# Kernel tuning notes

Hardware: AMD Instinct MI355X
Metric: run time of the kernel (lower is better)

The kernel has to match this reference:

```python
import jax, jax.numpy as jnp
import numpy as np

NUM_SYMBOLS = 100000
EMBED_DIM = 256
DIM = 2 * EMBED_DIM          # 512
NUM_HEADS = 4
HEAD_DIM = DIM // NUM_HEADS  # 128
N = 100                      # hard-coded neighbor count in source
EPS = 1e-5


def layernorm(x, g, b):
    mu = jnp.mean(x, axis=-1, keepdims=True)
    var = jnp.var(x, axis=-1, keepdims=True)
    return (x - mu) * jax.lax.rsqrt(var + EPS) * g + b


def setup_inputs() -> dict:
    key = jax.random.key(0)
    ks = jax.random.split(key, 12)
    B, FEW = 512, 2
    connections = jax.random.randint(ks[0], (B, FEW, N, 2), 0, NUM_SYMBOLS)
    mask = jax.random.randint(ks[1], (B * FEW, N, N), 0, 2).astype(jnp.int32)
    s = 0.02
    emb = jax.random.normal(ks[2], (NUM_SYMBOLS + 1, EMBED_DIM), jnp.float32) * s
    qkv_w = jax.random.normal(ks[3], (3 * DIM, DIM), jnp.float32) * s
    qkv_b = jnp.zeros((3 * DIM,), jnp.float32)
    proj_w = jax.random.normal(ks[4], (DIM, DIM), jnp.float32) * s
    proj_b = jnp.zeros((DIM,), jnp.float32)
    ln1_g = jnp.ones((DIM,), jnp.float32); ln1_b = jnp.zeros((DIM,), jnp.float32)
    ln2_g = jnp.ones((DIM,), jnp.float32); ln2_b = jnp.zeros((DIM,), jnp.float32)
    fc_w = jax.random.normal(ks[5], (DIM // 2, DIM), jnp.float32) * s
    fc_b = jnp.zeros((DIM // 2,), jnp.float32)
    return {"connections": connections, "mask": mask, "emb": emb,
            "qkv_w": qkv_w, "qkv_b": qkv_b, "proj_w": proj_w, "proj_b": proj_b,
            "ln1_g": ln1_g, "ln1_b": ln1_b, "ln2_g": ln2_g, "ln2_b": ln2_b,
            "fc_w": fc_w, "fc_b": fc_b}


def reference(connections, mask, emb, qkv_w, qkv_b, proj_w, proj_b,
              ln1_g, ln1_b, ln2_g, ln2_b, fc_w, fc_b):
    # embedding gathers for (relation, entity) pairs
    rel = emb[connections[..., 0]]          # [B, few, N, E]
    ent = emb[connections[..., 1]]          # [B, few, N, E]
    x = jnp.concatenate([rel, ent], axis=-1).reshape(-1, N, DIM)  # [BN, N, C]
    m = mask.reshape(-1, N, N)

    xn = layernorm(x, ln1_g, ln1_b)
    qkv = xn @ qkv_w.T + qkv_b              # [BN, N, 3C]
    BN = xn.shape[0]
    qkv = qkv.reshape(BN, N, 3, NUM_HEADS, HEAD_DIM).transpose(2, 0, 3, 1, 4)
    q, k, v = qkv[0], qkv[1], qkv[2]        # [BN, H, N, hd]

    scale = HEAD_DIM ** -0.5
    attn = jnp.einsum('bhnd,bhmd->bhnm', q, k) * scale
    attn = jnp.where(m[:, None] == 0, -1e9, attn)
    attn = jax.nn.softmax(attn, axis=-1)    # [BN, H, N, N]

    y = jnp.einsum('bhnm,bhmd->bhnd', attn, v)
    y = y.transpose(0, 2, 1, 3).reshape(BN, N, DIM)
    y = y @ proj_w.T + proj_b               # [BN, N, C]

    # attn.mean(dim=2): mean over query axis -> [BN, H, N]; bmm with y
    wc = jnp.einsum('bhn,bnc->bhc', attn.mean(axis=2), y)   # [BN, H, C]
    out = layernorm(wc, ln2_g, ln2_b) @ fc_w.T + fc_b       # [BN, H, C//2]
    return out
```

## Files before the change

### kernel.cpp

```cpp
#include <hip/hip_runtime.h>
#include <stdint.h>

typedef __attribute__((ext_vector_type(8))) short bf16x8;
typedef __attribute__((ext_vector_type(4))) float f32x4;
typedef __attribute__((ext_vector_type(4))) unsigned int u32x4;
typedef __attribute__((ext_vector_type(4))) unsigned short u16x4;

typedef const void __attribute__((address_space(1))) gvoid_t;
typedef void __attribute__((address_space(3))) lvoid_t;

__device__ __forceinline__ unsigned short f2bf(float f) {
  union { float f; unsigned int u; } v; v.f = f;
  unsigned int u = v.u;
  u += 0x7fffu + ((u >> 16) & 1u);
  return (unsigned short)(u >> 16);
}
__device__ __forceinline__ float bf2f(unsigned short h) {
  union { unsigned int u; float f; } v; v.u = ((unsigned int)h) << 16;
  return v.f;
}
__device__ __forceinline__ void load_lds16(const void* g, void* l) {
  __builtin_amdgcn_global_load_lds((gvoid_t*)g, (lvoid_t*)l, 16, 0, 0);
}

#define GATE4() asm volatile("s_waitcnt vmcnt(4)" ::: "memory")
#define GATE0() asm volatile("s_waitcnt vmcnt(0)" ::: "memory")
#define BARRIER()                    \
  do {                               \
    asm volatile("" ::: "memory");   \
    __builtin_amdgcn_s_barrier();    \
    asm volatile("" ::: "memory");   \
  } while (0)

__global__ __launch_bounds__(256) void k_cvt(const float* __restrict__ src,
                                             unsigned short* __restrict__ dst, int n) {
  int i = blockIdx.x * 256 + threadIdx.x;
  if (i < n) dst[i] = f2bf(src[i]);
}

__global__ __launch_bounds__(256) void k_maskpack(const int* __restrict__ mask,
                                                  unsigned int* __restrict__ bm) {
  const int lane = threadIdx.x & 63;
  const int wv = (blockIdx.x << 2) + (threadIdx.x >> 6);
  const int r0 = wv * 16;
  for (int i = 0; i < 16; ++i) {
    const int r = r0 + i;
    const size_t base = (size_t)r * 100;
    const int c0 = mask[base + lane];
    int c1 = 0;
    if (lane < 36) c1 = mask[base + 64 + lane];
    const unsigned long long b0 = __ballot(c0 != 0);
    const unsigned long long b1 = __ballot(c1 != 0);
    if (lane == 0) {
      u32x4 v;
      v[0] = (unsigned int)b0; v[1] = (unsigned int)(b0 >> 32);
      v[2] = (unsigned int)b1; v[3] = (unsigned int)(b1 >> 32);
      *(u32x4*)(bm + (size_t)r * 4) = v;
    }
  }
}

__global__ __launch_bounds__(256) void k_gather_ln(const int* __restrict__ conn,
                                                   const float* __restrict__ emb,
                                                   const float* __restrict__ g1,
                                                   const float* __restrict__ b1,
                                                   unsigned short* __restrict__ xn,
                                                   int row0) {
  const int lane = threadIdx.x & 63;
  const int wid = threadIdx.x >> 6;
  const int rloc = blockIdx.x * 4 + wid;
  const int row = row0 + rloc;
  const int rel = conn[row * 2 + 0];
  const int ent = conn[row * 2 + 1];
  const float4 r4 = *(const float4*)(emb + (size_t)rel * 256 + lane * 4);
  const float4 e4 = *(const float4*)(emb + (size_t)ent * 256 + lane * 4);
  float rv[4] = {r4.x, r4.y, r4.z, r4.w};
  float ev[4] = {e4.x, e4.y, e4.z, e4.w};
  float s = 0.f, ss = 0.f;
#pragma unroll
  for (int j = 0; j < 4; ++j) { s += rv[j] + ev[j]; ss += rv[j] * rv[j] + ev[j] * ev[j]; }
#pragma unroll
  for (int d = 1; d < 64; d <<= 1) { s += __shfl_xor(s, d, 64); ss += __shfl_xor(ss, d, 64); }
  const float mu = s * (1.f / 512.f);
  const float var = ss * (1.f / 512.f) - mu * mu;
  const float rs = rsqrtf(var + 1e-5f);
  const float4 ga = *(const float4*)(g1 + lane * 4);
  const float4 gb = *(const float4*)(g1 + 256 + lane * 4);
  const float4 ba = *(const float4*)(b1 + lane * 4);
  const float4 bb = *(const float4*)(b1 + 256 + lane * 4);
  float gav[4] = {ga.x, ga.y, ga.z, ga.w}, gbv[4] = {gb.x, gb.y, gb.z, gb.w};
  float bav[4] = {ba.x, ba.y, ba.z, ba.w}, bbv[4] = {bb.x, bb.y, bb.z, bb.w};
  u16x4 o0, o1;
#pragma unroll
  for (int j = 0; j < 4; ++j) {
    o0[j] = f2bf((rv[j] - mu) * rs * gav[j] + bav[j]);
    o1[j] = f2bf((ev[j] - mu) * rs * gbv[j] + bbv[j]);
  }
  unsigned short* orow = xn + (size_t)rloc * 512;
  *(u16x4*)(orow + lane * 4) = o0;
  *(u16x4*)(orow + 256 + lane * 4) = o1;
}

template <typename CT>
__global__ __launch_bounds__(256) void k_gemm3(const unsigned short* __restrict__ A,
                                               const unsigned short* __restrict__ W,
                                               const float* __restrict__ bias,
                                               CT* __restrict__ C,
                                               int N, int K, int ntiles, int nwg) {
  __shared__ __align__(16) unsigned short ldsA[3][128 * 32];
  __shared__ __align__(16) unsigned short ldsB[3][128 * 32];

  const int orig = blockIdx.x;
  const int q = nwg >> 3, r = nwg & 7;
  const int xcd = orig & 7, idx = orig >> 3;
  const int wg = (xcd < r ? xcd * (q + 1) : r * (q + 1) + (xcd - r) * q) + idx;
  const int mtile = wg / ntiles, ntile = wg % ntiles;

  const int t = threadIdx.x, lane = t & 63, wid = t >> 6;
  const int wm = wid >> 1, wn = wid & 1;
  const size_t Abase = (size_t)mtile * 128 * K;
  const size_t Wbase = (size_t)ntile * 128 * K;
  const int NT = K >> 5;

  f32x4 acc[4][4];
#pragma unroll
  for (int i = 0; i < 4; ++i)
#pragma unroll
    for (int j = 0; j < 4; ++j) acc[i][j] = (f32x4){0.f, 0.f, 0.f, 0.f};

  const int sr0 = t >> 2;
  auto stage = [&](int buf, int kt) {
#pragma unroll
    for (int it = 0; it < 2; ++it) {
      const int row = it * 64 + sr0;
      const int cl = (t & 3) ^ ((row >> 1) & 3);
      load_lds16(A + Abase + (size_t)row * K + kt * 32 + cl * 8, &ldsA[buf][it * 2048 + t * 8]);
    }
#pragma unroll
    for (int it = 0; it < 2; ++it) {
      const int row = it * 64 + sr0;
      const int cl = (t & 3) ^ ((row >> 1) & 3);
      load_lds16(W + Wbase + (size_t)row * K + kt * 32 + cl * 8, &ldsB[buf][it * 2048 + t * 8]);
    }
  };

  stage(0, 0);
  stage(1, 1);

  int cur = 0;
  for (int kt = 0; kt < NT; ++kt) {
    if (kt + 1 < NT) { GATE4(); } else { GATE0(); }
    BARRIER();
    if (kt + 2 < NT) {
      int s2 = cur + 2; if (s2 >= 3) s2 -= 3;
      stage(s2, kt + 2);
    }
    bf16x8 af[4], bfr[4];
#pragma unroll
    for (int mi = 0; mi < 4; ++mi) {
      const int row = wm * 64 + mi * 16 + (lane & 15);
      const int st = (lane >> 4) ^ ((row >> 1) & 3);
      af[mi] = *(const bf16x8*)&ldsA[cur][row * 32 + st * 8];
    }
#pragma unroll
    for (int ni = 0; ni < 4; ++ni) {
      const int row = wn * 64 + ni * 16 + (lane & 15);
      const int st = (lane >> 4) ^ ((row >> 1) & 3);
      bfr[ni] = *(const bf16x8*)&ldsB[cur][row * 32 + st * 8];
    }
#pragma unroll
    for (int mi = 0; mi < 4; ++mi)
#pragma unroll
      for (int ni = 0; ni < 4; ++ni)
        acc[mi][ni] = __builtin_amdgcn_mfma_f32_16x16x32_bf16(af[mi], bfr[ni], acc[mi][ni], 0, 0, 0);
    cur = (cur + 1 == 3) ? 0 : cur + 1;
  }

#pragma unroll
  for (int ni = 0; ni < 4; ++ni) {
    const int col = ntile * 128 + wn * 64 + ni * 16 + (lane & 15);
    const float bv = bias[col];
#pragma unroll
    for (int mi = 0; mi < 4; ++mi) {
      const int row0 = mtile * 128 + wm * 64 + mi * 16 + ((lane >> 4) << 2);
#pragma unroll
      for (int r2 = 0; r2 < 4; ++r2) {
        const float ov = acc[mi][ni][r2] + bv;
        if constexpr (sizeof(CT) == 2)
          C[(size_t)(row0 + r2) * N + col] = (CT)f2bf(ov);
        else
          C[(size_t)(row0 + r2) * N + col] = (CT)ov;
      }
    }
  }
}

__global__ __launch_bounds__(512) void k_attn(const unsigned short* __restrict__ qkv,
                                              const unsigned int* __restrict__ bm,
                                              unsigned short* __restrict__ y,
                                              float* __restrict__ am, int b0) {
  __shared__ __align__(16) unsigned short A_lds[128 * 128];
  __shared__ __align__(16) unsigned short P_lds[7 * 16 * 128];
  __shared__ float am_s[112];
  const int t = threadIdx.x, lane = t & 63, w = t >> 6;
  const int bl = blockIdx.x >> 2, h = blockIdx.x & 3;
  const int bg = b0 + bl;
  const unsigned short* qk = qkv + (size_t)bl * 153600;

  if (t < 112) am_s[t] = 0.f;

#pragma unroll
  for (int j = 0; j < 4; ++j) {
    const int row = j * 32 + w * 4 + (lane >> 4);
    if (row < 100) {
      const int c = (lane & 15) ^ (row & 7);
      load_lds16(qk + (size_t)row * 1536 + 512 + h * 128 + c * 8,
                 &A_lds[j * 4096 + w * 512 + lane * 8]);
    }
  }
  u32x4 vv[4];
#pragma unroll
  for (int p = 0; p < 4; ++p) {
    const int vm = p * 32 + (t >> 4);
    const u32x4 z = {0u, 0u, 0u, 0u};
    vv[p] = (vm < 100) ? *(const u32x4*)(qk + (size_t)vm * 1536 + 1024 + h * 128 + (t & 15) * 8) : z;
  }
  bf16x8 qf[4];
  {
    const int qrow = w * 16 + (lane & 15);
    const bool qv = (w < 7) && (qrow < 100);
#pragma unroll
    for (int kk = 0; kk < 4; ++kk) {
      const bf16x8 z = {0, 0, 0, 0, 0, 0, 0, 0};
      qf[kk] = qv ? *(const bf16x8*)(qk + (size_t)qrow * 1536 + h * 128 + kk * 32 + (lane >> 4) * 8) : z;
    }
  }
  if (t < 192) {
    const u32x4 z = {0u, 0u, 0u, 0u};
    *(u32x4*)&A_lds[(100 + (t >> 4)) * 128 + (t & 15) * 8] = z;
  }
  __syncthreads();

  f32x4 sa[7];
#pragma unroll
  for (int ni = 0; ni < 7; ++ni) sa[ni] = (f32x4){0.f, 0.f, 0.f, 0.f};
  if (w < 7) {
#pragma unroll
    for (int kk = 0; kk < 4; ++kk)
#pragma unroll
      for (int ni = 0; ni < 7; ++ni) {
        const int row = ni * 16 + (lane & 15);
        const int c = (kk * 4 + (lane >> 4)) ^ (row & 7);
        const bf16x8 kf = *(const bf16x8*)&A_lds[row * 128 + (c << 3)];
        sa[ni] = __builtin_amdgcn_mfma_f32_16x16x32_bf16(qf[kk], kf, sa[ni], 0, 0, 0);
      }
  }
  __syncthreads();

#pragma unroll
  for (int p = 0; p < 4; ++p) {
    const int vm = p * 32 + (t >> 4);
    unsigned short tmp[8];
    *(u32x4*)tmp = vv[p];
#pragma unroll
    for (int jj = 0; jj < 8; ++jj) {
      const int d = (lane & 15) * 8 + jj;
      const int swz = (vm >> 3) ^ (((d >> 3) ^ d) & 7);
      A_lds[d * 128 + swz * 8 + (vm & 7)] = tmp[jj];
    }
  }

  if (w < 7) {
    const float scale = 0.08838834764831843f;
    float psum[7] = {0.f, 0.f, 0.f, 0.f, 0.f, 0.f, 0.f};
#pragma unroll
    for (int r = 0; r < 4; ++r) {
      const int lr = (lane >> 4) * 4 + r;
      const int qrow = w * 16 + lr;
      if (qrow < 100) {
        const u32x4 bmv = *(const u32x4*)(bm + ((size_t)bg * 100 + qrow) * 4);
        float x[7];
#pragma unroll
        for (int ni = 0; ni < 7; ++ni) {
          const int col = ni * 16 + (lane & 15);
          const unsigned int bit = (bmv[ni >> 1] >> (((ni & 1) << 4) + (lane & 15))) & 1u;
          x[ni] = (col < 100) ? (bit ? sa[ni][r] * scale : -1e9f) : -1e30f;
        }
        float mx = x[0];
#pragma unroll
        for (int ni = 1; ni < 7; ++ni) mx = fmaxf(mx, x[ni]);
#pragma unroll
        for (int dd = 1; dd < 16; dd <<= 1) mx = fmaxf(mx, __shfl_xor(mx, dd, 64));
        float e[7], sum = 0.f;
#pragma unroll
        for (int ni = 0; ni < 7; ++ni) { e[ni] = __expf(x[ni] - mx); sum += e[ni]; }
#pragma unroll
        for (int dd = 1; dd < 16; dd <<= 1) sum += __shfl_xor(sum, dd, 64);
        const float inv = 1.f / sum;
#pragma unroll
        for (int ni = 0; ni < 7; ++ni) {
          const float pv = e[ni] * inv;
          psum[ni] += pv;
          const int col = ni * 16 + (lane & 15);
          const int c = (col >> 3) ^ (lr & 7);
          P_lds[w * 2048 + lr * 128 + c * 8 + (col & 7)] = f2bf(pv);
        }
      } else {
#pragma unroll
        for (int ni = 0; ni < 7; ++ni) {
          const int col = ni * 16 + (lane & 15);
          const int c = (col >> 3) ^ (lr & 7);
          P_lds[w * 2048 + lr * 128 + c * 8 + (col & 7)] = 0;
        }
      }
    }
    if (lane < 32) {
      const int lr = lane & 15;
      const int c = (14 + (lane >> 4)) ^ (lr & 7);
      const u32x4 z = {0u, 0u, 0u, 0u};
      *(u32x4*)&P_lds[w * 2048 + lr * 128 + c * 8] = z;
    }
#pragma unroll
    for (int ni = 0; ni < 7; ++ni) atomicAdd(&am_s[ni * 16 + (lane & 15)], psum[ni]);
  }
  __syncthreads();

  if (t < 100) am[((size_t)bg * 4 + h) * 100 + t] = am_s[t] * 0.01f;

  if (w < 7) {
#pragma unroll
    for (int dt = 0; dt < 8; ++dt) {
      f32x4 acc = {0.f, 0.f, 0.f, 0.f};
#pragma unroll
      for (int kk = 0; kk < 4; ++kk) {
        const int c = kk * 4 + (lane >> 4);
        const bf16x8 pf = *(const bf16x8*)&P_lds[w * 2048 + (lane & 15) * 128 + ((c ^ (lane & 7)) << 3)];
        const int d = dt * 16 + (lane & 15);
        const int cv = c ^ (((d >> 3) ^ d) & 7);
        const bf16x8 vf = *(const bf16x8*)&A_lds[d * 128 + (cv << 3)];
        acc = __builtin_amdgcn_mfma_f32_16x16x32_bf16(pf, vf, acc, 0, 0, 0);
      }
      const int d = dt * 16 + (lane & 15);
#pragma unroll
      for (int r = 0; r < 4; ++r) {
        const int qrow = w * 16 + (lane >> 4) * 4 + r;
        if (qrow < 100)
          y[((size_t)bl * 100 + qrow) * 512 + h * 128 + d] = f2bf(acc[r]);
      }
    }
  }
}

__global__ __launch_bounds__(256) void k_z(const float* __restrict__ am,
                                           const unsigned short* __restrict__ y,
                                           unsigned short* __restrict__ zb, int b0) {
  __shared__ float ams[400];
  const int bl = blockIdx.x, t = threadIdx.x;
  const int bg = b0 + bl;
  for (int i = t; i < 400; i += 256) ams[i] = am[(size_t)bg * 400 + i];
  __syncthreads();
  float a0[4] = {0, 0, 0, 0}, a1[4] = {0, 0, 0, 0};
  const unsigned short* yb = y + (size_t)bl * 100 * 512 + t * 2;
  for (int n = 0; n < 100; ++n) {
    const unsigned int u = *(const unsigned int*)(yb + (size_t)n * 512);
    const float v0 = bf2f((unsigned short)(u & 0xffffu));
    const float v1 = bf2f((unsigned short)(u >> 16));
#pragma unroll
    for (int hh = 0; hh < 4; ++hh) {
      const float ww = ams[hh * 100 + n];
      a0[hh] += ww * v0;
      a1[hh] += ww * v1;
    }
  }
#pragma unroll
  for (int hh = 0; hh < 4; ++hh) {
    const unsigned int pk = (unsigned int)f2bf(a0[hh]) | ((unsigned int)f2bf(a1[hh]) << 16);
    *(unsigned int*)(zb + ((size_t)(bl * 4 + hh)) * 512 + 2 * t) = pk;
  }
}

__global__ __launch_bounds__(256) void k_ln2(const unsigned short* __restrict__ wcb,
                                             const float* __restrict__ g2,
                                             const float* __restrict__ b2,
                                             unsigned short* __restrict__ wcn) {
  const int t = threadIdx.x, lane = t & 63, w = t >> 6;
  const int row = blockIdx.x * 4 + w;
  const u32x4 pv = *(const u32x4*)(wcb + (size_t)row * 512 + lane * 8);
  float v[8];
#pragma unroll
  for (int j = 0; j < 4; ++j) {
    v[2 * j] = bf2f((unsigned short)(pv[j] & 0xffffu));
    v[2 * j + 1] = bf2f((unsigned short)(pv[j] >> 16));
  }
  float s = 0.f, ss = 0.f;
#pragma unroll
  for (int j = 0; j < 8; ++j) { s += v[j]; ss += v[j] * v[j]; }
#pragma unroll
  for (int d = 1; d < 64; d <<= 1) { s += __shfl_xor(s, d, 64); ss += __shfl_xor(ss, d, 64); }
  const float mu = s * (1.f / 512.f);
  const float var = ss * (1.f / 512.f) - mu * mu;
  const float rs = rsqrtf(var + 1e-5f);
  const float4 ga = *(const float4*)(g2 + lane * 8);
  const float4 gb = *(const float4*)(g2 + lane * 8 + 4);
  const float4 ba = *(const float4*)(b2 + lane * 8);
  const float4 bb = *(const float4*)(b2 + lane * 8 + 4);
  const float gv[8] = {ga.x, ga.y, ga.z, ga.w, gb.x, gb.y, gb.z, gb.w};
  const float bv[8] = {ba.x, ba.y, ba.z, ba.w, bb.x, bb.y, bb.z, bb.w};
  u32x4 ov;
#pragma unroll
  for (int j = 0; j < 4; ++j) {
    const unsigned short lo = f2bf((v[2 * j] - mu) * rs * gv[2 * j] + bv[2 * j]);
    const unsigned short hi = f2bf((v[2 * j + 1] - mu) * rs * gv[2 * j + 1] + bv[2 * j + 1]);
    ov[j] = (unsigned int)lo | ((unsigned int)hi << 16);
  }
  *(u32x4*)(wcn + (size_t)row * 512 + lane * 8) = ov;
}

extern "C" void kernel_launch(void* const* d_in, const int* in_sizes, int n_in,
                              void* d_out, int out_size, void* d_ws, size_t ws_size,
                              hipStream_t stream) {
  const int* conn = (const int*)d_in[0];
  const int* mask = (const int*)d_in[1];
  const float* emb = (const float*)d_in[2];
  const float* qkv_w = (const float*)d_in[3];
  const float* qkv_b = (const float*)d_in[4];
  const float* proj_w = (const float*)d_in[5];
  const float* proj_b = (const float*)d_in[6];
  const float* ln1g = (const float*)d_in[7];
  const float* ln1b = (const float*)d_in[8];
  const float* ln2g = (const float*)d_in[9];
  const float* ln2b = (const float*)d_in[10];
  const float* fc_w = (const float*)d_in[11];
  const float* fc_b = (const float*)d_in[12];
  float* out = (float*)d_out;

  size_t off = 0;
  auto alloc = [&](size_t bytes) {
    void* p = (char*)d_ws + off;
    off += (bytes + 255) & ~(size_t)255;
    return p;
  };
  unsigned short* w_qkv = (unsigned short*)alloc((size_t)1536 * 512 * 2);
  unsigned short* w_proj = (unsigned short*)alloc((size_t)512 * 512 * 2);
  unsigned short* w_fc = (unsigned short*)alloc((size_t)256 * 512 * 2);
  float* am = (float*)alloc((size_t)1024 * 400 * 4);
  unsigned int* bmb = (unsigned int*)alloc((size_t)102400 * 16);
  const size_t fixed = off;

  int CB = 512;
  while (CB > 64) {
    size_t need = fixed + (size_t)CB * 4 * 512 * 2 * 3 + (size_t)CB * 100 * 512 * 2 +
                  (size_t)CB * 100 * 1536 * 2 + 4096;
    if (need <= ws_size) break;
    CB >>= 1;
  }
  unsigned short* zbuf = (unsigned short*)alloc((size_t)CB * 4 * 512 * 2);
  unsigned short* wcb = (unsigned short*)alloc((size_t)CB * 4 * 512 * 2);
  unsigned short* wcn = (unsigned short*)alloc((size_t)CB * 4 * 512 * 2);
  unsigned short* xn = (unsigned short*)alloc((size_t)CB * 100 * 512 * 2);
  unsigned short* qkvb = (unsigned short*)alloc((size_t)CB * 100 * 1536 * 2);

  k_cvt<<<(786432 + 255) / 256, 256, 0, stream>>>(qkv_w, w_qkv, 786432);
  k_cvt<<<(262144 + 255) / 256, 256, 0, stream>>>(proj_w, w_proj, 262144);
  k_cvt<<<(131072 + 255) / 256, 256, 0, stream>>>(fc_w, w_fc, 131072);
  k_maskpack<<<1600, 256, 0, stream>>>(mask, bmb);

  for (int b0 = 0; b0 < 1024; b0 += CB) {
    const int mt = CB * 100 / 128;
    const int zt = CB * 4 / 128;
    k_gather_ln<<<CB * 25, 256, 0, stream>>>(conn, emb, ln1g, ln1b, xn, b0 * 100);
    k_gemm3<unsigned short><<<12 * mt, 256, 0, stream>>>(xn, w_qkv, qkv_b, qkvb, 1536, 512, 12, 12 * mt);
    k_attn<<<CB * 4, 512, 0, stream>>>(qkvb, bmb, xn , am, b0);
    k_z<<<CB, 256, 0, stream>>>(am, xn , zbuf, b0);
    k_gemm3<unsigned short><<<4 * zt, 256, 0, stream>>>(zbuf, w_proj, proj_b, wcb, 512, 512, 4, 4 * zt);
    k_ln2<<<CB, 256, 0, stream>>>(wcb, ln2g, ln2b, wcn);
    k_gemm3<float><<<2 * zt, 256, 0, stream>>>(wcn, w_fc, fc_b, out + (size_t)b0 * 1024, 256, 512, 2, 2 * zt);
  }
}
```

Measured before the change: 546.8 us.

## Use 256x256 8-wave ping-pong GEMM for QKV, fuse weight casts, enlarge chunk

Replaces the 128x128 QKV GEMM with a 512-thread kernel that computes 256x256 output tiles. It uses double-buffered, swizzled LDS staging and interleaves global-to-LDS loads with MFMA phases under barriers and raised priority. The three weight conversion launches are merged into a single kernel, and the batch chunk size now starts at 1024 so fewer loop iterations and launches happen when workspace allows. The larger tiles raise operand reuse but need more LDS and registers, which lowers occupancy, and the bigger chunk needs more workspace.

```diff
diff --git a/kernel.cpp b/kernel.cpp
--- a/kernel.cpp
+++ b/kernel.cpp
@@ -32,10 +32,18 @@
     asm volatile("" ::: "memory");   \
   } while (0)
 
-__global__ __launch_bounds__(256) void k_cvt(const float* __restrict__ src,
-                                             unsigned short* __restrict__ dst, int n) {
+__global__ __launch_bounds__(256) void k_cvt3(const float* __restrict__ s0, int n0,
+                                              const float* __restrict__ s1, int n1,
+                                              const float* __restrict__ s2, int n2,
+                                              unsigned short* __restrict__ d0,
+                                              unsigned short* __restrict__ d1,
+                                              unsigned short* __restrict__ d2) {
   int i = blockIdx.x * 256 + threadIdx.x;
-  if (i < n) dst[i] = f2bf(src[i]);
+  if (i < n0) { d0[i] = f2bf(s0[i]); return; }
+  i -= n0;
+  if (i < n1) { d1[i] = f2bf(s1[i]); return; }
+  i -= n1;
+  if (i < n2) d2[i] = f2bf(s2[i]);
 }
 
 __global__ __launch_bounds__(256) void k_maskpack(const int* __restrict__ mask,
@@ -101,6 +109,133 @@
   *(u16x4*)(orow + 256 + lane * 4) = o1;
 }
 
+__global__ __launch_bounds__(512, 2) void k_gemm8(const unsigned short* __restrict__ A,
+                                                  const unsigned short* __restrict__ W,
+                                                  const float* __restrict__ bias,
+                                                  unsigned short* __restrict__ C,
+                                                  int N, int K, int ntiles, int nwg) {
+  __shared__ __align__(16) unsigned short ldsA[2][2][128 * 64];
+  __shared__ __align__(16) unsigned short ldsB[2][2][128 * 64];
+
+  const int orig = blockIdx.x;
+  const int q = nwg >> 3, rr = nwg & 7;
+  const int xcd = orig & 7, idx = orig >> 3;
+  const int wg = (xcd < rr ? xcd * (q + 1) : rr * (q + 1) + (xcd - rr) * q) + idx;
+  const int mtile = wg / ntiles, ntile = wg % ntiles;
+
+  const int t = threadIdx.x, lane = t & 63, wid = t >> 6;
+  const int wm = wid >> 2, wn = wid & 3;
+  const size_t Abase = (size_t)mtile * 256 * K;
+  const size_t Wbase = (size_t)ntile * 256 * K;
+  const int NT = K >> 6;
+  const int G = NT >> 1;
+
+  const int lr0 = t >> 3;
+  const int g0 = t & 7;
+  auto stageA = [&](int bb, int h, int kt) {
+#pragma unroll
+    for (int L = 0; L < 2; ++L) {
+      const int lr = L * 64 + lr0;
+      const int gs = g0 ^ (lr & 7);
+      load_lds16(A + Abase + (size_t)(h * 128 + lr) * K + kt * 64 + gs * 8,
+                 &ldsA[bb][h][L * 4096 + t * 8]);
+    }
+  };
+  auto stageB = [&](int bb, int h, int kt) {
+#pragma unroll
+    for (int L = 0; L < 2; ++L) {
+      const int lr = L * 64 + lr0;
+      const int gs = g0 ^ (lr & 7);
+      load_lds16(W + Wbase + (size_t)(h * 128 + lr) * K + kt * 64 + gs * 8,
+                 &ldsB[bb][h][L * 4096 + t * 8]);
+    }
+  };
+
+  f32x4 acc[8][4];
+#pragma unroll
+  for (int i = 0; i < 8; ++i)
+#pragma unroll
+    for (int j = 0; j < 4; ++j) acc[i][j] = (f32x4){0.f, 0.f, 0.f, 0.f};
+
+  bf16x8 afL[8], afH[8], bf01[4], bf23[4];
+  const int la = lane & 15, ls = lane >> 4;
+
+  auto rdA = [&](int bb, int mibase, bf16x8* dst) {
+#pragma unroll
+    for (int m2 = 0; m2 < 4; ++m2)
+#pragma unroll
+      for (int kk = 0; kk < 2; ++kk) {
+        const int lr = (mibase + m2) * 16 + la;
+        const int g = (kk * 4 + ls) ^ (lr & 7);
+        dst[m2 * 2 + kk] = *(const bf16x8*)&ldsA[bb][wm][lr * 64 + g * 8];
+      }
+  };
+  auto rdB = [&](int bb, int nibase, bf16x8* dst) {
+#pragma unroll
+    for (int n2 = 0; n2 < 2; ++n2)
+#pragma unroll
+      for (int kk = 0; kk < 2; ++kk) {
+        const int lrb = (wn & 1) * 64 + (nibase + n2) * 16 + la;
+        const int g = (kk * 4 + ls) ^ (lrb & 7);
+        dst[n2 * 2 + kk] = *(const bf16x8*)&ldsB[bb][wn >> 1][lrb * 64 + g * 8];
+      }
+  };
+  auto mm = [&](const bf16x8* af, const bf16x8* bf, int mibase, int nibase) {
+    __builtin_amdgcn_s_setprio(1);
+#pragma unroll
+    for (int m2 = 0; m2 < 4; ++m2)
+#pragma unroll
+      for (int n2 = 0; n2 < 2; ++n2)
+#pragma unroll
+        for (int kk = 0; kk < 2; ++kk)
+          acc[mibase + m2][nibase + n2] = __builtin_amdgcn_mfma_f32_16x16x32_bf16(
+              af[m2 * 2 + kk], bf[n2 * 2 + kk], acc[mibase + m2][nibase + n2], 0, 0, 0);
+    __builtin_amdgcn_s_setprio(0);
+  };
+
+  stageA(0, 0, 0); stageA(0, 1, 0); stageB(0, 0, 0); stageB(0, 1, 0);
+  stageA(1, 0, 1); stageA(1, 1, 1);
+  GATE4();
+  BARRIER();
+
+  for (int g = 0; g < G; ++g) {
+    const int v = 2 * g + 1;
+    int w0 = 2 * g + 2; if (w0 >= NT) w0 -= NT;
+    int w1 = 2 * g + 3; if (w1 >= NT) w1 -= NT;
+    rdA(0, 0, afL); rdB(0, 0, bf01); stageB(1, 0, v);
+    BARRIER(); mm(afL, bf01, 0, 0); BARRIER();
+    rdA(0, 4, afH); stageB(1, 1, v);
+    BARRIER(); mm(afH, bf01, 4, 0); BARRIER();
+    rdB(0, 2, bf23); stageA(0, 0, w0);
+    BARRIER(); mm(afH, bf23, 4, 2); BARRIER();
+    stageA(0, 1, w0);
+    GATE4();
+    BARRIER(); mm(afL, bf23, 0, 2); BARRIER();
+    rdA(1, 0, afL); rdB(1, 0, bf01); stageB(0, 0, w0);
+    BARRIER(); mm(afL, bf01, 0, 0); BARRIER();
+    rdA(1, 4, afH); stageB(0, 1, w0);
+    BARRIER(); mm(afH, bf01, 4, 0); BARRIER();
+    rdB(1, 2, bf23); stageA(1, 0, w1);
+    BARRIER(); mm(afH, bf23, 4, 2); BARRIER();
+    stageA(1, 1, w1);
+    GATE4();
+    BARRIER(); mm(afL, bf23, 0, 2); BARRIER();
+  }
+
+#pragma unroll
+  for (int ni = 0; ni < 4; ++ni) {
+    const int col = ntile * 256 + wn * 64 + ni * 16 + la;
+    const float bv = bias[col];
+#pragma unroll
+    for (int mi = 0; mi < 8; ++mi) {
+      const int row0 = mtile * 256 + wm * 128 + mi * 16 + ls * 4;
+#pragma unroll
+      for (int r2 = 0; r2 < 4; ++r2)
+        C[(size_t)(row0 + r2) * N + col] = f2bf(acc[mi][ni][r2] + bv);
+    }
+  }
+}
+
 template <typename CT>
 __global__ __launch_bounds__(256) void k_gemm3(const unsigned short* __restrict__ A,
                                                const unsigned short* __restrict__ W,
@@ -447,10 +582,10 @@
   unsigned int* bmb = (unsigned int*)alloc((size_t)102400 * 16);
   const size_t fixed = off;
 
-  int CB = 512;
+  int CB = 1024;
   while (CB > 64) {
     size_t need = fixed + (size_t)CB * 4 * 512 * 2 * 3 + (size_t)CB * 100 * 512 * 2 +
-                  (size_t)CB * 100 * 1536 * 2 + 4096;
+                  (size_t)CB * 100 * 1536 * 2 + 8192;
     if (need <= ws_size) break;
     CB >>= 1;
   }
@@ -460,16 +595,15 @@
   unsigned short* xn = (unsigned short*)alloc((size_t)CB * 100 * 512 * 2);
   unsigned short* qkvb = (unsigned short*)alloc((size_t)CB * 100 * 1536 * 2);
 
-  k_cvt<<<(786432 + 255) / 256, 256, 0, stream>>>(qkv_w, w_qkv, 786432);
-  k_cvt<<<(262144 + 255) / 256, 256, 0, stream>>>(proj_w, w_proj, 262144);
-  k_cvt<<<(131072 + 255) / 256, 256, 0, stream>>>(fc_w, w_fc, 131072);
+  k_cvt3<<<(786432 + 262144 + 131072 + 255) / 256, 256, 0, stream>>>(
+      qkv_w, 786432, proj_w, 262144, fc_w, 131072, w_qkv, w_proj, w_fc);
   k_maskpack<<<1600, 256, 0, stream>>>(mask, bmb);
 
   for (int b0 = 0; b0 < 1024; b0 += CB) {
-    const int mt = CB * 100 / 128;
+    const int mt256 = CB * 100 / 256;
     const int zt = CB * 4 / 128;
     k_gather_ln<<<CB * 25, 256, 0, stream>>>(conn, emb, ln1g, ln1b, xn, b0 * 100);
-    k_gemm3<unsigned short><<<12 * mt, 256, 0, stream>>>(xn, w_qkv, qkv_b, qkvb, 1536, 512, 12, 12 * mt);
+    k_gemm8<<<6 * mt256, 512, 0, stream>>>(xn, w_qkv, qkv_b, qkvb, 1536, 512, 6, 6 * mt256);
     k_attn<<<CB * 4, 512, 0, stream>>>(qkvb, bmb, xn , am, b0);
     k_z<<<CB, 256, 0, stream>>>(am, xn , zbuf, b0);
     k_gemm3<unsigned short><<<4 * zt, 256, 0, stream>>>(zbuf, w_proj, proj_b, wcb, 512, 512, 4, 4 * zt);
```

After: 570.1 us. +4.3%, slower.
